# Performance work log

Hardware: AMD Instinct MI355X
Metric: run time of the kernel (lower is better)

The kernel has to match this reference:

```python
import jax, jax.numpy as jnp
import numpy as np

N_INST = 8  # max instance id; ids 1..N_INST, 0 = background
MESH_NORM = 1024.0  # from SegmantationLoss._meshgrid


def _meshgrid(H, W):
    y = jnp.arange(H, dtype=jnp.float32) / MESH_NORM
    x = jnp.arange(W, dtype=jnp.float32) / MESH_NORM
    return jnp.stack([jnp.broadcast_to(y[:, None], (H, W)),
                      jnp.broadcast_to(x[None, :], (H, W))], axis=0)  # [2,H,W]


def _lovasz_hinge_batch(logits, labels, delta=1.0):
    """logits, labels: [K,P] float. Returns [K] lovasz hinge losses."""
    signs = 2.0 * labels - 1.0
    errors = delta - logits * signs
    order = jnp.argsort(-errors, axis=1)  # descending
    es = jnp.take_along_axis(errors, order, axis=1)
    gs = jnp.take_along_axis(labels, order, axis=1)
    gts = gs.sum(axis=1, keepdims=True)
    intersection = gts - jnp.cumsum(gs, axis=1)
    union = gts + jnp.cumsum(1.0 - gs, axis=1)
    jac = 1.0 - intersection / union
    grad = jnp.concatenate([jac[:, :1], jac[:, 1:] - jac[:, :-1]], axis=1)
    return (jax.nn.relu(es) * grad).sum(axis=1)


def setup_inputs() -> dict:
    key = jax.random.key(0)
    k1, k2, k3, k4 = jax.random.split(key, 4)
    B, H, W = 4, 512, 1024
    x_vec = jax.random.normal(k1, (B, 2, H, W), dtype=jnp.float32)
    # small scale so psigma = exp(10*ppsigma) stays in a sane range
    x_sigma = jax.random.normal(k2, (B, 2, H, W), dtype=jnp.float32) * 0.03
    x_seed = jax.random.normal(k3, (B, 1, H, W), dtype=jnp.float32)
    t = jax.random.randint(k4, (B, H, W), 0, 9, dtype=jnp.int32)
    return {"x_vec": x_vec, "x_sigma": x_sigma, "x_seed": x_seed, "t": t}


def reference(x_vec, x_sigma, x_seed, t):
    B, _, H, W = x_vec.shape
    mesh = _meshgrid(H, W)

    emb = jnp.tanh(x_vec) + mesh[None]          # [B,2,H,W] spatial embedding
    ppsig = x_sigma                              # [B,2,H,W] pre-pseudo-sigma
    seed = jax.nn.sigmoid(x_seed)[:, 0]          # [B,H,W]

    ids = jnp.arange(1, N_INST + 1, dtype=t.dtype)
    mf = (t[None] == ids[:, None, None, None]).astype(jnp.float32)  # [N,B,H,W]
    cnt = mf.sum(axis=(2, 3))                    # [N,B]
    present = cnt > 0
    safe = jnp.maximum(cnt, 1.0)
    n_present = jnp.maximum(present.sum(axis=0).astype(jnp.float32), 1.0)  # [B]

    # per-instance masked means
    centroid = jnp.einsum('nbhw,bchw->nbc', mf, emb) / safe[..., None]    # [N,B,2]
    inst_pps = jnp.einsum('nbhw,bchw->nbc', mf, ppsig) / safe[..., None]  # [N,B,2]
    psigma = jnp.exp(10.0 * inst_pps)                                     # [N,B,2]

    # gaussian between pixel and instance embedding (l22n)
    diff2 = (emb[None] - centroid[..., None, None]) ** 2                  # [N,B,2,H,W]
    dist = (diff2 * psigma[..., None, None]).sum(axis=2)                  # [N,B,H,W]
    gauss = jnp.exp(-0.5 * dist)                                          # [N,B,H,W]

    # lovasz hinge per instance on logits 2*gauss - 1 over all pixels
    P = H * W
    lov = _lovasz_hinge_batch((2.0 * gauss - 1.0).reshape(N_INST * B, P),
                              mf.reshape(N_INST * B, P)).reshape(N_INST, B)
    lov = jnp.where(present, lov, 0.0)
    lovasz_loss = (lov.sum(axis=0) / n_present).mean()

    # sigma loss: pixel ppsigma -> detached instance mean ppsigma
    sd = (ppsig[None] - jax.lax.stop_gradient(inst_pps)[..., None, None]) ** 2
    sl = (sd.sum(axis=2) * mf).sum(axis=(2, 3)) / safe                    # [N,B]
    sl = jnp.where(present, sl, 0.0)
    sigma_loss = (sl.sum(axis=0) / n_present).mean()

    # seed loss: background -> 0, foreground -> detached gaussian
    bg = (t == 0).astype(jnp.float32)                                     # [B,H,W]
    bg_cnt = jnp.maximum(bg.sum(axis=(1, 2)), 1.0)
    bg_loss = ((seed ** 2) * bg).sum(axis=(1, 2)) / bg_cnt                # [B]
    fg = ((seed[None] - jax.lax.stop_gradient(gauss)) ** 2 * mf).sum(axis=(2, 3)) / safe
    fg = jnp.where(present, fg, 0.0)
    seed_loss = ((bg_loss + fg.sum(axis=0)) /
                 (1.0 + present.sum(axis=0).astype(jnp.float32))).mean()

    return lovasz_loss + sigma_loss + seed_loss
```

## Files before the change

kernel.cpp:

```cpp
#include <hip/hip_runtime.h>
#include <math.h>

#define B 4
#define H 512
#define W 1024
#define P (H*W)
#define NI 8
#define NSEG 32
#define NB 256
#define NSTRIP 256
#define STRIP_PX (P/NSTRIP)
#define K1B 128
#define K1PX (P/K1B)

#define D_CYP  0
#define D_CXP  32
#define D_AY   64
#define D_AX   96
#define D_CNT  128
#define D_SL   160
#define D_K4C  192
#define OFF_FGP 256
#define OFF_HIST (OFF_FGP + 9*1024)
#define OFF_FOLD (OFF_HIST + NSEG*NSTRIP*NB)
#define OFF_PK1  (OFF_FOLD + 8*NSEG*NB)

__device__ __forceinline__ float fast_tanh(float x) {
    float e = __expf(2.0f * x);
    return 1.0f - 2.0f / (e + 1.0f);
}
__device__ __forceinline__ float fast_sigmoid(float x) {
    return 1.0f / (1.0f + __expf(-x));
}
template<int CTRL, int RM>
__device__ __forceinline__ float dpp_add(float x) {
    int y = __builtin_amdgcn_update_dpp(0, __float_as_int(x), CTRL, RM, 0xF, true);
    return x + __int_as_float(y);
}
__device__ __forceinline__ float wred(float x) {
    x = dpp_add<0x111, 0xF>(x);
    x = dpp_add<0x112, 0xF>(x);
    x = dpp_add<0x114, 0xF>(x);
    x = dpp_add<0x118, 0xF>(x);
    x = dpp_add<0x142, 0xA>(x);
    x = dpp_add<0x143, 0xC>(x);
    return x;
}

__global__ __launch_bounds__(256) void k1_stats(const float* __restrict__ xv,
                                                const float* __restrict__ xs,
                                                const int*  __restrict__ t,
                                                float* __restrict__ pk1) {
    const int b = blockIdx.y, bx = blockIdx.x, tid = threadIdx.x;
    const int lane = tid & 63, wid = tid >> 6;
    const float* xv_y = xv + (size_t)b*2*P;
    const float* xv_x = xv_y + P;
    const float* xs_y = xs + (size_t)b*2*P;
    const float* xs_x = xs_y + P;
    const int*   tb   = t + (size_t)b*P;

    float cnt[NI], sey[NI], sex[NI], sgy[NI], sgx[NI], sq[NI];
    #pragma unroll
    for (int n = 0; n < NI; ++n) { cnt[n]=0.f; sey[n]=0.f; sex[n]=0.f; sgy[n]=0.f; sgx[n]=0.f; sq[n]=0.f; }

    #pragma unroll
    for (int it = 0; it < 4; ++it) {
        int p0 = bx*K1PX + it*1024 + tid*4;
        float4 vy = *(const float4*)(xv_y + p0);
        float4 vx = *(const float4*)(xv_x + p0);
        float4 sy = *(const float4*)(xs_y + p0);
        float4 sx = *(const float4*)(xs_x + p0);
        int4   tt = *(const int4*)(tb + p0);
        #pragma unroll
        for (int j = 0; j < 4; ++j) {
            int pix = p0 + j;
            float ey = fast_tanh((&vy.x)[j]) + (float)(pix >> 10) * (1.0f/1024.0f);
            float ex = fast_tanh((&vx.x)[j]) + (float)(pix & 1023) * (1.0f/1024.0f);
            float gy = (&sy.x)[j], gx = (&sx.x)[j];
            int tv = (&tt.x)[j];
            float q = gy*gy + gx*gx;
            #pragma unroll
            for (int n = 0; n < NI; ++n) {
                float m = (tv == n+1) ? 1.0f : 0.0f;
                cnt[n] += m; sey[n] += m*ey; sex[n] += m*ex;
                sgy[n] += m*gy; sgx[n] += m*gx; sq[n] += m*q;
            }
        }
    }
    __shared__ float sw[4*64];
    #define RED48(val, slot) { float r_ = wred(val); if (lane == 63) sw[wid*64 + (slot)] = r_; }
    #pragma unroll
    for (int n = 0; n < NI; ++n) {
        RED48(cnt[n], n*6+0); RED48(sey[n], n*6+1); RED48(sex[n], n*6+2);
        RED48(sgy[n], n*6+3); RED48(sgx[n], n*6+4); RED48(sq[n],  n*6+5);
    }
    #undef RED48
    __syncthreads();
    if (tid < 48) {
        float s = sw[tid] + sw[64+tid] + sw[128+tid] + sw[192+tid];
        pk1[(size_t)(b*K1B + bx)*64 + tid] = s;
    }
}

__global__ __launch_bounds__(1024) void k2_finalize(float* __restrict__ wsf,
                                                    const float* __restrict__ pk1,
                                                    float* __restrict__ out) {
    const int tid = threadIdx.x;
    __shared__ float part[16*64];
    __shared__ float ssum[4*64];
    const int v = tid & 63, g = tid >> 6;
    const int b = g >> 2, c = g & 3;
    float acc = 0.f;
    const int jbase = b*K1B + c*32;
    #pragma unroll 8
    for (int i = 0; i < 32; ++i) acc += pk1[(size_t)(jbase + i)*64 + v];
    part[g*64 + v] = acc;
    __syncthreads();
    if (tid < 256) {
        int vb = tid & 63, bb = tid >> 6;
        ssum[bb*64+vb] = part[(bb*4+0)*64+vb] + part[(bb*4+1)*64+vb]
                       + part[(bb*4+2)*64+vb] + part[(bb*4+3)*64+vb];
    }
    __syncthreads();
    if (tid < NSEG) {
        int n = tid >> 2, bb = tid & 3;
        float cv  = ssum[bb*64 + n*6+0];
        float sey = ssum[bb*64 + n*6+1];
        float sex = ssum[bb*64 + n*6+2];
        float sgy = ssum[bb*64 + n*6+3];
        float sgx = ssum[bb*64 + n*6+4];
        float sq  = ssum[bb*64 + n*6+5];
        float safe = fmaxf(cv, 1.0f);
        float ipy = sgy/safe, ipx = sgx/safe;
        float ceny = sey/safe, cenx = sex/safe;
        const float hl2e = 0.7213475204444817f;
        float ay = sqrtf(expf(10.0f*ipy) * hl2e);
        float ax = sqrtf(expf(10.0f*ipx) * hl2e);
        wsf[D_AY+tid]  = ay;
        wsf[D_AX+tid]  = ax;
        wsf[D_CYP+tid] = ay*ceny;
        wsf[D_CXP+tid] = ax*cenx;
        wsf[D_CNT+tid] = cv;
        wsf[D_SL+tid]  = sq/safe - (ipy*ipy + ipx*ipx);
    } else if (tid < 64) {
        ((unsigned*)wsf)[D_K4C + (tid - 32)] = 0u;
    } else if (tid == 64) {
        out[0] = 0.f;
    }
}

__global__ __launch_bounds__(512) void k3_hist(const float* __restrict__ xv,
                                               const float* __restrict__ xseed,
                                               const int*  __restrict__ t,
                                               const float* __restrict__ wsf,
                                               unsigned* __restrict__ hist_g,
                                               float* __restrict__ fgp) {
    const int strip = blockIdx.x;
    const int b     = blockIdx.y;
    const int tid   = threadIdx.x;
    const int lane  = tid & 63;

    __shared__ unsigned hist[NI*NB];
    *((uint4*)hist + tid) = (uint4){0u,0u,0u,0u};
    __shared__ float spar[4*NI];
    if (tid < 4*NI) {
        int n = tid & (NI-1), q = tid >> 3;
        spar[tid] = wsf[q*32 + n*B + b];
    }
    __syncthreads();

    float cyp[NI], cxp[NI], ay[NI], ax[NI], fgn[NI];
    #pragma unroll
    for (int n = 0; n < NI; ++n) {
        cyp[n] = spar[n]; cxp[n] = spar[NI+n];
        ay[n] = spar[2*NI+n]; ax[n] = spar[3*NI+n];
        fgn[n] = 0.f;
    }
    float bgq = 0.f;

    const float* xv_y = xv + (size_t)b*2*P;
    const float* xv_x = xv_y + P;
    const float* sdp  = xseed + (size_t)b*P;
    const int*   tb   = t + (size_t)b*P;

    {
        int p0 = strip * STRIP_PX + tid*4;
        float4 vy = *(const float4*)(xv_y + p0);
        float4 vx = *(const float4*)(xv_x + p0);
        float4 se = *(const float4*)(sdp + p0);
        int4   tt = *(const int4*)(tb + p0);
        #pragma unroll
        for (int j = 0; j < 4; ++j) {
            int pix = p0 + j;
            float ey = fast_tanh((&vy.x)[j]) + (float)(pix >> 10) * (1.0f/1024.0f);
            float ex = fast_tanh((&vx.x)[j]) + (float)(pix & 1023) * (1.0f/1024.0f);
            int tv = (&tt.x)[j];
            float gown = 0.f;
            #pragma unroll
            for (int n = 0; n < NI; ++n) {
                float dyp = fmaf(ey, ay[n], -cyp[n]);
                float dxp = fmaf(ex, ax[n], -cxp[n]);
                float e = fmaf(dxp, dxp, dyp*dyp);
                float kg = exp2f(8.0f - e);
                bool lab = (tv == n+1);
                float sel = lab ? (256.0f - kg) : kg;
                int key = (int)sel;
                key = key > (NB-1) ? (NB-1) : key;
                if (key > 0) atomicAdd(&hist[n*NB + key], lab ? 0x10000u : 1u);
                if (lab) gown = kg * 0.00390625f;
            }
            float s = fast_sigmoid((&se.x)[j]);
            if (tv > 0) {
                float d = s - gown;
                float dd = d*d;
                #pragma unroll
                for (int n = 0; n < NI; ++n) fgn[n] += (tv == n+1) ? dd : 0.f;
            } else {
                bgq += s*s;
            }
        }
    }
    __syncthreads();
    {
        int lin = tid*4;
        int n = lin >> 8, key = lin & (NB-1);
        uint4 v = *(const uint4*)&hist[lin];
        *(uint4*)&hist_g[((size_t)((n*4 + b)*NSTRIP + strip))*NB + key] = v;
    }
    __shared__ float sfg[NI+1];
    if (tid < NI+1) sfg[tid] = 0.f;
    __syncthreads();
    #pragma unroll
    for (int n = 0; n < NI; ++n) {
        float r = wred(fgn[n]);
        if (lane == 63 && r != 0.f) atomicAdd(&sfg[n], r);
    }
    {
        float r = wred(bgq);
        if (lane == 63) atomicAdd(&sfg[NI], r);
    }
    __syncthreads();
    if (tid < NI+1) fgp[tid*1024 + b*NSTRIP + strip] = sfg[tid];
}

__global__ __launch_bounds__(256) void k4_fused(const unsigned* __restrict__ hist_g,
                                                unsigned* __restrict__ fold,
                                                float* __restrict__ wsf,
                                                const float* __restrict__ fgp,
                                                float* __restrict__ out) {
    const int q = blockIdx.x;
    const int seg = blockIdx.y;
    const int tid = threadIdx.x;

    unsigned posk, negk;
    {
        const unsigned* src = hist_g + (size_t)(seg*NSTRIP + q*64)*NB + tid;
        unsigned pos = 0u, neg = 0u;
        #pragma unroll 8
        for (int s = 0; s < 64; ++s) {
            unsigned v = src[(size_t)s*NB];
            pos += v >> 16; neg += v & 0xffffu;
        }
        fold[((size_t)q*NSEG + seg)*NB + tid] = pos;
        fold[(size_t)4*NSEG*NB + ((size_t)q*NSEG + seg)*NB + tid] = neg;
        posk = pos; negk = neg;
    }

    __shared__ unsigned slast;
    __syncthreads();
    if (tid == 0) {
        __threadfence();
        unsigned* cnt4 = (unsigned*)wsf + D_K4C;
        slast = __hip_atomic_fetch_add(&cnt4[seg], 1u, __ATOMIC_ACQ_REL,
                                       __HIP_MEMORY_SCOPE_AGENT);
    }
    __syncthreads();
    if (slast != 3u) return;
    __threadfence();

    const int n = seg >> 2, b = seg & 3;
    __shared__ float scnt[NSEG];
    __shared__ float sfr[256];
    __shared__ unsigned up[256], un[256];
    __shared__ double sdd[256];
    if (tid < NSEG) scnt[tid] = wsf[D_CNT + tid];
    __syncthreads();

    if (n == 0) {
        sfr[tid] = fgp[NI*1024 + b*NSTRIP + tid];
        __syncthreads();
        #pragma unroll
        for (int d = 128; d > 0; d >>= 1) {
            if (tid < d) sfr[tid] += sfr[tid + d];
            __syncthreads();
        }
        if (tid == 0) {
            float bgs = sfr[0];
            int np = 0; float ss = 0.f, csum = 0.f;
            for (int k = 0; k < NI; ++k) {
                float cv = scnt[k*4 + b];
                csum += cv;
                if (cv > 0.5f) { np++; ss += wsf[D_SL + k*4 + b]; }
            }
            float bgc = fmaxf((float)P - csum, 1.0f);
            float bgl = bgs / bgc;
            float npf = fmaxf((float)np, 1.0f);
            atomicAdd(out, (ss/npf + bgl/(1.0f + (float)np)) * (1.0f/(float)B));
        }
        __syncthreads();
    }

    const float G = scnt[seg];
    if (G < 0.5f) return;
    int npc = 0;
    #pragma unroll
    for (int k = 0; k < NI; ++k) npc += (scnt[k*4 + b] > 0.5f) ? 1 : 0;

    sfr[tid] = fgp[n*1024 + b*NSTRIP + tid];
    __syncthreads();
    #pragma unroll
    for (int d = 128; d > 0; d >>= 1) {
        if (tid < d) sfr[tid] += sfr[tid + d];
        __syncthreads();
    }
    const float FG = sfr[0];

    unsigned pos = posk, neg = negk;
    #pragma unroll
    for (int qq = 0; qq < 4; ++qq) {
        if (qq == q) continue;
        pos += fold[((size_t)qq*NSEG + seg)*NB + tid];
        neg += fold[(size_t)4*NSEG*NB + ((size_t)qq*NSEG + seg)*NB + tid];
    }

    up[tid] = pos; un[tid] = neg;
    __syncthreads();
    for (int d = 1; d < 256; d <<= 1) {
        unsigned ap = (tid + d < 256) ? up[tid + d] : 0u;
        unsigned an = (tid + d < 256) ? un[tid + d] : 0u;
        __syncthreads();
        up[tid] += ap; un[tid] += an;
        __syncthreads();
    }
    const unsigned TP = up[0], TN = un[0];
    const unsigned Gu = (unsigned)(G + 0.5f);
    const unsigned NEGu = (unsigned)P - Gu;
    unsigned cump = up[tid] - pos;
    unsigned cumn = un[tid] - neg;

    const double dG = (double)G;
    double acc = 0.0;
    {
        unsigned cp = pos, cn = neg;
        if (tid == 0) { cp = Gu - TP; cn = NEGu - TN; }
        if (cp | cn) {
            unsigned ep = cump, en = cumn;
            unsigned epi = ep + cp, eni = en + cn;
            double jb = 1.0 - (dG - (double)ep)  / (dG + (double)en);
            double ja = 1.0 - (dG - (double)epi) / (dG + (double)eni);
            acc = (((double)tid + 0.5) * (2.0/(double)NB)) * (ja - jb);
        }
    }
    sdd[tid] = acc;
    __syncthreads();
    #pragma unroll
    for (int d = 128; d > 0; d >>= 1) {
        if (tid < d) sdd[tid] += sdd[tid + d];
        __syncthreads();
    }
    if (tid == 0) {
        float npf = fmaxf((float)npc, 1.0f);
        float val = (float)sdd[0] / (npf * (float)B)
                  + (FG / G) / ((1.0f + (float)npc) * (float)B);
        atomicAdd(out, val);
    }
}

extern "C" void kernel_launch(void* const* d_in, const int* in_sizes, int n_in,
                              void* d_out, int out_size, void* d_ws, size_t ws_size,
                              hipStream_t stream) {
    (void)in_sizes; (void)n_in; (void)out_size; (void)ws_size;
    const float* xv  = (const float*)d_in[0];
    const float* xs  = (const float*)d_in[1];
    const float* xsd = (const float*)d_in[2];
    const int*   t   = (const int*)d_in[3];
    float* wsf = (float*)d_ws;
    unsigned* hist_g = (unsigned*)d_ws + OFF_HIST;
    unsigned* fold   = (unsigned*)d_ws + OFF_FOLD;
    float* pk1 = wsf + OFF_PK1;
    float* fgp = wsf + OFF_FGP;
    float* out = (float*)d_out;

    k1_stats<<<dim3(K1B, B), 256, 0, stream>>>(xv, xs, t, pk1);
    k2_finalize<<<1, 1024, 0, stream>>>(wsf, pk1, out);
    k3_hist<<<dim3(NSTRIP, B), 512, 0, stream>>>(xv, xsd, t, wsf, hist_g, fgp);
    k4_fused<<<dim3(4, NSEG), 256, 0, stream>>>(hist_g, fold, wsf, fgp, out);
}
```

Baseline: 128.6 us.

## Remove finalize kernel by recomputing per-instance stats in consumer kernels

Result: no change. 127.8 us (-0.6%).

```diff
diff --git a/kernel.cpp b/kernel.cpp
--- a/kernel.cpp
+++ b/kernel.cpp
@@ -13,14 +13,8 @@
 #define K1B 128
 #define K1PX (P/K1B)
 
-#define D_CYP  0
-#define D_CXP  32
-#define D_AY   64
-#define D_AX   96
-#define D_CNT  128
-#define D_SL   160
-#define D_K4C  192
-#define OFF_FGP 256
+#define D_K4C  0
+#define OFF_FGP 64
 #define OFF_HIST (OFF_FGP + 9*1024)
 #define OFF_FOLD (OFF_HIST + NSEG*NSTRIP*NB)
 #define OFF_PK1  (OFF_FOLD + 8*NSEG*NB)
@@ -50,9 +44,15 @@
 __global__ __launch_bounds__(256) void k1_stats(const float* __restrict__ xv,
                                                 const float* __restrict__ xs,
                                                 const int*  __restrict__ t,
-                                                float* __restrict__ pk1) {
+                                                float* __restrict__ pk1,
+                                                unsigned* __restrict__ wsu,
+                                                float* __restrict__ out) {
     const int b = blockIdx.y, bx = blockIdx.x, tid = threadIdx.x;
     const int lane = tid & 63, wid = tid >> 6;
+    if (bx == 0 && b == 0) {
+        if (tid < 32) wsu[D_K4C + tid] = 0u;
+        else if (tid == 32) out[0] = 0.f;
+    }
     const float* xv_y = xv + (size_t)b*2*P;
     const float* xv_x = xv_y + P;
     const float* xs_y = xs + (size_t)b*2*P;
@@ -102,57 +102,10 @@
     }
 }
 
-__global__ __launch_bounds__(1024) void k2_finalize(float* __restrict__ wsf,
-                                                    const float* __restrict__ pk1,
-                                                    float* __restrict__ out) {
-    const int tid = threadIdx.x;
-    __shared__ float part[16*64];
-    __shared__ float ssum[4*64];
-    const int v = tid & 63, g = tid >> 6;
-    const int b = g >> 2, c = g & 3;
-    float acc = 0.f;
-    const int jbase = b*K1B + c*32;
-    #pragma unroll 8
-    for (int i = 0; i < 32; ++i) acc += pk1[(size_t)(jbase + i)*64 + v];
-    part[g*64 + v] = acc;
-    __syncthreads();
-    if (tid < 256) {
-        int vb = tid & 63, bb = tid >> 6;
-        ssum[bb*64+vb] = part[(bb*4+0)*64+vb] + part[(bb*4+1)*64+vb]
-                       + part[(bb*4+2)*64+vb] + part[(bb*4+3)*64+vb];
-    }
-    __syncthreads();
-    if (tid < NSEG) {
-        int n = tid >> 2, bb = tid & 3;
-        float cv  = ssum[bb*64 + n*6+0];
-        float sey = ssum[bb*64 + n*6+1];
-        float sex = ssum[bb*64 + n*6+2];
-        float sgy = ssum[bb*64 + n*6+3];
-        float sgx = ssum[bb*64 + n*6+4];
-        float sq  = ssum[bb*64 + n*6+5];
-        float safe = fmaxf(cv, 1.0f);
-        float ipy = sgy/safe, ipx = sgx/safe;
-        float ceny = sey/safe, cenx = sex/safe;
-        const float hl2e = 0.7213475204444817f;
-        float ay = sqrtf(expf(10.0f*ipy) * hl2e);
-        float ax = sqrtf(expf(10.0f*ipx) * hl2e);
-        wsf[D_AY+tid]  = ay;
-        wsf[D_AX+tid]  = ax;
-        wsf[D_CYP+tid] = ay*ceny;
-        wsf[D_CXP+tid] = ax*cenx;
-        wsf[D_CNT+tid] = cv;
-        wsf[D_SL+tid]  = sq/safe - (ipy*ipy + ipx*ipx);
-    } else if (tid < 64) {
-        ((unsigned*)wsf)[D_K4C + (tid - 32)] = 0u;
-    } else if (tid == 64) {
-        out[0] = 0.f;
-    }
-}
-
 __global__ __launch_bounds__(512) void k3_hist(const float* __restrict__ xv,
                                                const float* __restrict__ xseed,
                                                const int*  __restrict__ t,
-                                               const float* __restrict__ wsf,
+                                               const float* __restrict__ pk1,
                                                unsigned* __restrict__ hist_g,
                                                float* __restrict__ fgp) {
     const int strip = blockIdx.x;
@@ -161,12 +114,43 @@
     const int lane  = tid & 63;
 
     __shared__ unsigned hist[NI*NB];
+    __shared__ float sred[8*64];
+    __shared__ float spar[4*NI];
+
+    {
+        const int v = tid & 63, g = tid >> 6;
+        float acc = 0.f;
+        const float* base = pk1 + (size_t)(b*K1B + g*16)*64 + v;
+        #pragma unroll
+        for (int i = 0; i < 16; ++i) acc += base[(size_t)i*64];
+        sred[g*64 + v] = acc;
+        __syncthreads();
+        if (tid < 64) {
+            float s = 0.f;
+            #pragma unroll
+            for (int g2 = 0; g2 < 8; ++g2) s += sred[g2*64 + tid];
+            sred[tid] = s;
+        }
+        __syncthreads();
+        if (tid < NI) {
+            int n = tid;
+            float cv  = sred[n*6+0];
+            float sey = sred[n*6+1];
+            float sex = sred[n*6+2];
+            float sgy = sred[n*6+3];
+            float sgx = sred[n*6+4];
+            float safe = fmaxf(cv, 1.0f);
+            float ipy = sgy/safe, ipx = sgx/safe;
+            const float hl2e = 0.7213475204444817f;
+            float ayv = sqrtf(expf(10.0f*ipy) * hl2e);
+            float axv = sqrtf(expf(10.0f*ipx) * hl2e);
+            spar[n]      = ayv*(sey/safe);
+            spar[NI+n]   = axv*(sex/safe);
+            spar[2*NI+n] = ayv;
+            spar[3*NI+n] = axv;
+        }
+    }
     *((uint4*)hist + tid) = (uint4){0u,0u,0u,0u};
-    __shared__ float spar[4*NI];
-    if (tid < 4*NI) {
-        int n = tid & (NI-1), q = tid >> 3;
-        spar[tid] = wsf[q*32 + n*B + b];
-    }
     __syncthreads();
 
     float cyp[NI], cxp[NI], ay[NI], ax[NI], fgn[NI];
@@ -245,12 +229,42 @@
 
 __global__ __launch_bounds__(256) void k4_fused(const unsigned* __restrict__ hist_g,
                                                 unsigned* __restrict__ fold,
-                                                float* __restrict__ wsf,
+                                                const float* __restrict__ pk1,
+                                                unsigned* __restrict__ wsu,
                                                 const float* __restrict__ fgp,
                                                 float* __restrict__ out) {
     const int q = blockIdx.x;
     const int seg = blockIdx.y;
     const int tid = threadIdx.x;
+    const int n = seg >> 2, b = seg & 3;
+
+    __shared__ float sred4[4*64];
+    __shared__ float scnt8[NI], ssl8[NI];
+    {
+        const int v = tid & 63, g = tid >> 6;
+        float acc = 0.f;
+        const float* base = pk1 + (size_t)(b*K1B + g*32)*64 + v;
+        #pragma unroll
+        for (int i = 0; i < 32; ++i) acc += base[(size_t)i*64];
+        sred4[g*64 + v] = acc;
+        __syncthreads();
+        if (tid < 64) {
+            float s = sred4[tid] + sred4[64+tid] + sred4[128+tid] + sred4[192+tid];
+            sred4[tid] = s;
+        }
+        __syncthreads();
+        if (tid < NI) {
+            float cv  = sred4[tid*6+0];
+            float sgy = sred4[tid*6+3];
+            float sgx = sred4[tid*6+4];
+            float sq  = sred4[tid*6+5];
+            float safe = fmaxf(cv, 1.0f);
+            float ipy = sgy/safe, ipx = sgx/safe;
+            scnt8[tid] = cv;
+            ssl8[tid]  = sq/safe - (ipy*ipy + ipx*ipx);
+        }
+        __syncthreads();
+    }
 
     unsigned posk, negk;
     {
@@ -270,21 +284,16 @@
     __syncthreads();
     if (tid == 0) {
         __threadfence();
-        unsigned* cnt4 = (unsigned*)wsf + D_K4C;
-        slast = __hip_atomic_fetch_add(&cnt4[seg], 1u, __ATOMIC_ACQ_REL,
+        slast = __hip_atomic_fetch_add(&wsu[D_K4C + seg], 1u, __ATOMIC_ACQ_REL,
                                        __HIP_MEMORY_SCOPE_AGENT);
     }
     __syncthreads();
     if (slast != 3u) return;
     __threadfence();
 
-    const int n = seg >> 2, b = seg & 3;
-    __shared__ float scnt[NSEG];
     __shared__ float sfr[256];
     __shared__ unsigned up[256], un[256];
     __shared__ double sdd[256];
-    if (tid < NSEG) scnt[tid] = wsf[D_CNT + tid];
-    __syncthreads();
 
     if (n == 0) {
         sfr[tid] = fgp[NI*1024 + b*NSTRIP + tid];
@@ -298,9 +307,9 @@
             float bgs = sfr[0];
             int np = 0; float ss = 0.f, csum = 0.f;
             for (int k = 0; k < NI; ++k) {
-                float cv = scnt[k*4 + b];
+                float cv = scnt8[k];
                 csum += cv;
-                if (cv > 0.5f) { np++; ss += wsf[D_SL + k*4 + b]; }
+                if (cv > 0.5f) { np++; ss += ssl8[k]; }
             }
             float bgc = fmaxf((float)P - csum, 1.0f);
             float bgl = bgs / bgc;
@@ -310,11 +319,11 @@
         __syncthreads();
     }
 
-    const float G = scnt[seg];
+    const float G = scnt8[n];
     if (G < 0.5f) return;
     int npc = 0;
     #pragma unroll
-    for (int k = 0; k < NI; ++k) npc += (scnt[k*4 + b] > 0.5f) ? 1 : 0;
+    for (int k = 0; k < NI; ++k) npc += (scnt8[k] > 0.5f) ? 1 : 0;
 
     sfr[tid] = fgp[n*1024 + b*NSTRIP + tid];
     __syncthreads();
@@ -384,15 +393,14 @@
     const float* xs  = (const float*)d_in[1];
     const float* xsd = (const float*)d_in[2];
     const int*   t   = (const int*)d_in[3];
-    float* wsf = (float*)d_ws;
-    unsigned* hist_g = (unsigned*)d_ws + OFF_HIST;
-    unsigned* fold   = (unsigned*)d_ws + OFF_FOLD;
-    float* pk1 = wsf + OFF_PK1;
-    float* fgp = wsf + OFF_FGP;
+    unsigned* wsu = (unsigned*)d_ws;
+    unsigned* hist_g = wsu + OFF_HIST;
+    unsigned* fold   = wsu + OFF_FOLD;
+    float* pk1 = (float*)d_ws + OFF_PK1;
+    float* fgp = (float*)d_ws + OFF_FGP;
     float* out = (float*)d_out;
 
-    k1_stats<<<dim3(K1B, B), 256, 0, stream>>>(xv, xs, t, pk1);
-    k2_finalize<<<1, 1024, 0, stream>>>(wsf, pk1, out);
-    k3_hist<<<dim3(NSTRIP, B), 512, 0, stream>>>(xv, xsd, t, wsf, hist_g, fgp);
-    k4_fused<<<dim3(4, NSEG), 256, 0, stream>>>(hist_g, fold, wsf, fgp, out);
-}
+    k1_stats<<<dim3(K1B, B), 256, 0, stream>>>(xv, xs, t, pk1, wsu, out);
+    k3_hist<<<dim3(NSTRIP, B), 512, 0, stream>>>(xv, xsd, t, pk1, hist_g, fgp);
+    k4_fused<<<dim3(4, NSEG), 256, 0, stream>>>(hist_g, fold, pk1, wsu, fgp, out);
+}
```
